# Kernel tuning notes

Measured on AMD Instinct MI355X. Metric: run time of the kernel, lower is better.

The kernel has to match this reference:

```python
import jax, jax.numpy as jnp
import numpy as np

PC_RANGE = (0.0, -40.0, -3.0, 70.4, 40.0, 1.0)
N, C, M, L = 200000, 64, 50000, 2000000
H = W = 176  # bev grid bound for synthetic pillar indices


def setup_inputs() -> dict:
    key = jax.random.key(0)
    k1, k2, k3, k4, k5, k6 = jax.random.split(key, 6)
    # points live in relative coords in [0, range_extent)
    ext = jnp.array([PC_RANGE[3] - PC_RANGE[0], PC_RANGE[4] - PC_RANGE[1], PC_RANGE[5] - PC_RANGE[2]], jnp.float32)
    xyz = jax.random.uniform(k1, (N, 3), jnp.float32) * ext
    point_features = jax.random.normal(k2, (N, C), jnp.float32)
    pillar_centers = jax.random.uniform(k3, (M, 3), jnp.float32) * ext
    pillar_indices = jax.random.randint(k4, (M, 3), 0, H, jnp.int32)
    point_set_indices = jax.random.randint(k5, (L,), 0, N, jnp.int32)
    pillar_set_indices = jnp.sort(jax.random.randint(k6, (L,), 0, M, jnp.int32))
    return {
        "xyz": xyz,
        "point_features": point_features,
        "pillar_centers": pillar_centers,
        "pillar_indices": pillar_indices,
        "point_set_indices": point_set_indices,
        "pillar_set_indices": pillar_set_indices,
    }


def reference(xyz, point_features, pillar_centers, pillar_indices, point_set_indices, pillar_set_indices):
    # gather per-pair features / coords
    group_point_features = jnp.take(point_features, point_set_indices, axis=0)   # (L, C)
    group_point_xyz = jnp.take(xyz, point_set_indices, axis=0)                   # (L, 3)
    group_pillar_centers = jnp.take(pillar_centers, pillar_set_indices, axis=0)  # (L, 3)
    # offset of each point from its pillar center (relative coords)
    rel = group_point_xyz - group_pillar_centers                                 # (L, 3)
    # shift point coords to absolute frame
    offset = jnp.array([PC_RANGE[0], PC_RANGE[1], PC_RANGE[2]], group_point_xyz.dtype)
    absl = group_point_xyz + offset                                              # (L, 3)
    group_features = jnp.concatenate([group_point_features, absl, rel], axis=1)  # (L, C+6)
    indice2bev = jnp.ones((1,), jnp.float32)  # bev_flag=False path
    return pillar_indices, pillar_set_indices, group_features, indice2bev
```

## Files before the change

kernel.cpp:

```cpp
#include <hip/hip_runtime.h>

constexpr int       kM = 50000;
constexpr long long kL = 2000000;
constexpr int       kRowLen = 70;

constexpr long long kOutPillarIdx = 0;
constexpr long long kOutPsi       = 150000;
constexpr long long kOutGF        = 2150000;
constexpr long long kOutBev       = 142150000;

constexpr int kRowsPerWave = 16;
constexpr int kWaves       = 4;
constexpr int kTileRows    = kRowsPerWave * kWaves;
constexpr int kGrid        = (int)(kL / kTileRows);
constexpr int kPillarIdx4  = kM * 3 / 4;

__global__ __launch_bounds__(256, 8)
void pillar_group_fused_kernel(const float* __restrict__ xyz,
                               const float4* __restrict__ pf4,
                               const float* __restrict__ pc,
                               const int4*  __restrict__ pillar_idx4,
                               const int4*  __restrict__ psi4,
                               const int*   __restrict__ point_set_idx,
                               const int*   __restrict__ pillar_set_idx,
                               float* __restrict__ out) {
    const int tid  = threadIdx.x;
    const int wave = tid >> 6;
    const int lane = tid & 63;
    const int row0 = blockIdx.x * kTileRows + wave * kRowsPerWave;

    if (tid < 16) {
        int k = blockIdx.x * 16 + tid;
        int4 v = psi4[k];
        ((float4*)(out + kOutPsi))[k] =
            make_float4((float)v.x, (float)v.y, (float)v.z, (float)v.w);
    } else if (tid == 16) {
        int k = blockIdx.x;
        if (k < kPillarIdx4) {
            int4 v = pillar_idx4[k];
            ((float4*)(out + kOutPillarIdx))[k] =
                make_float4((float)v.x, (float)v.y, (float)v.z, (float)v.w);
        }
    } else if (tid == 17) {
        int k = kGrid + blockIdx.x;
        if (k < kPillarIdx4) {
            int4 v = pillar_idx4[k];
            ((float4*)(out + kOutPillarIdx))[k] =
                make_float4((float)v.x, (float)v.y, (float)v.z, (float)v.w);
        }
    } else if (tid == 18 && blockIdx.x == 0) {
        out[kOutBev] = 1.0f;
    }

    int idxv = 0;
    if (lane < 16)       idxv = point_set_idx[row0 + lane];
    else if (lane < 32)  idxv = pillar_set_idx[row0 + lane - 16];

    float* gf = out + kOutGF;

    {
        const int j    = lane & 15;
        const int rsub = lane >> 4;
        #pragma unroll
        for (int it = 0; it < 4; ++it) {
            const int r = it * 4 + rsub;
            const int p = __shfl(idxv, r);
            const float4 v = pf4[(long long)p * 16 + j];
            float* dst = gf + (long long)(row0 + r) * kRowLen + j * 4;
            *(float2*)(dst)     = make_float2(v.x, v.y);
            *(float2*)(dst + 2) = make_float2(v.z, v.w);
        }
    }

    if (lane < kRowsPerWave * 3) {
        const int r = lane / 3;
        const int c = lane - r * 3;
        const int p = __shfl(idxv, r);
        const int q = __shfl(idxv, 16 + r);
        const float x   = xyz[(long long)p * 3 + c];
        const float pcv = pc[(long long)q * 3 + c];
        const float off = (c == 0) ? 0.0f : ((c == 1) ? -40.0f : -3.0f);
        float* rowp = gf + (long long)(row0 + r) * kRowLen;
        rowp[64 + c] = x + off;
        rowp[67 + c] = x - pcv;
    }
}

extern "C" void kernel_launch(void* const* d_in, const int* in_sizes, int n_in,
                              void* d_out, int out_size, void* d_ws, size_t ws_size,
                              hipStream_t stream) {
    const float* xyz             = (const float*)d_in[0];
    const float* point_features  = (const float*)d_in[1];
    const float* pillar_centers  = (const float*)d_in[2];
    const int*   pillar_indices  = (const int*)d_in[3];
    const int*   point_set_idx   = (const int*)d_in[4];
    const int*   pillar_set_idx  = (const int*)d_in[5];

    float* out = (float*)d_out;

    pillar_group_fused_kernel<<<kGrid, 256, 0, stream>>>(
        xyz, (const float4*)point_features, pillar_centers,
        (const int4*)pillar_indices, (const int4*)pillar_set_idx,
        point_set_idx, pillar_set_idx, out);
}
```

Before: 238.2 us.

## Stage gathered rows in LDS via direct global-to-LDS loads, then store as float4

Point-feature rows are now gathered straight into shared memory with global_load_lds, and the xyz/rel columns are written to LDS as well. Each wave then writes its 16x70 output tile as contiguous 16-byte stores instead of scattered float2 and scalar stores. The aim is fully coalesced, aligned wide writes on a store-bound kernel. In exchange it adds LDS usage, a full vmcnt wait, and per-element index arithmetic (division by 280) during the write-out.

```diff
diff --git a/kernel.cpp b/kernel.cpp
--- a/kernel.cpp
+++ b/kernel.cpp
@@ -15,6 +15,17 @@
 constexpr int kGrid        = (int)(kL / kTileRows);
 constexpr int kPillarIdx4  = kM * 3 / 4;
 
+constexpr int kAFloats    = kRowsPerWave * 64;
+constexpr int kBFloats    = kRowsPerWave * 6;
+constexpr int kWaveFloats = kAFloats + kBFloats;
+
+__device__ __forceinline__ void gload_lds16(const void* g, void* l) {
+    __builtin_amdgcn_global_load_lds(
+        (__attribute__((address_space(1))) void*)g,
+        (__attribute__((address_space(3))) void*)l,
+        16, 0, 0);
+}
+
 __global__ __launch_bounds__(256, 8)
 void pillar_group_fused_kernel(const float* __restrict__ xyz,
                                const float4* __restrict__ pf4,
@@ -24,10 +35,29 @@
                                const int*   __restrict__ point_set_idx,
                                const int*   __restrict__ pillar_set_idx,
                                float* __restrict__ out) {
+    __shared__ float s[kWaves * kWaveFloats];
+
     const int tid  = threadIdx.x;
     const int wave = tid >> 6;
     const int lane = tid & 63;
     const int row0 = blockIdx.x * kTileRows + wave * kRowsPerWave;
+    float* sA = &s[wave * kWaveFloats];
+    float* sB = sA + kAFloats;
+
+    int idxv = 0;
+    if (lane < 16)       idxv = point_set_idx[row0 + lane];
+    else if (lane < 32)  idxv = pillar_set_idx[row0 + lane - 16];
+
+    {
+        const int j    = lane & 15;
+        const int rsub = lane >> 4;
+        #pragma unroll
+        for (int it = 0; it < 4; ++it) {
+            const int r = it * 4 + rsub;
+            const int p = __shfl(idxv, r);
+            gload_lds16(&pf4[(long long)p * 16 + j], sA + it * 256);
+        }
+    }
 
     if (tid < 16) {
         int k = blockIdx.x * 16 + tid;
@@ -52,26 +82,6 @@
         out[kOutBev] = 1.0f;
     }
 
-    int idxv = 0;
-    if (lane < 16)       idxv = point_set_idx[row0 + lane];
-    else if (lane < 32)  idxv = pillar_set_idx[row0 + lane - 16];
-
-    float* gf = out + kOutGF;
-
-    {
-        const int j    = lane & 15;
-        const int rsub = lane >> 4;
-        #pragma unroll
-        for (int it = 0; it < 4; ++it) {
-            const int r = it * 4 + rsub;
-            const int p = __shfl(idxv, r);
-            const float4 v = pf4[(long long)p * 16 + j];
-            float* dst = gf + (long long)(row0 + r) * kRowLen + j * 4;
-            *(float2*)(dst)     = make_float2(v.x, v.y);
-            *(float2*)(dst + 2) = make_float2(v.z, v.w);
-        }
-    }
-
     if (lane < kRowsPerWave * 3) {
         const int r = lane / 3;
         const int c = lane - r * 3;
@@ -80,9 +90,32 @@
         const float x   = xyz[(long long)p * 3 + c];
         const float pcv = pc[(long long)q * 3 + c];
         const float off = (c == 0) ? 0.0f : ((c == 1) ? -40.0f : -3.0f);
-        float* rowp = gf + (long long)(row0 + r) * kRowLen;
-        rowp[64 + c] = x + off;
-        rowp[67 + c] = x - pcv;
+        sB[r * 6 + c]     = x + off;
+        sB[r * 6 + 3 + c] = x - pcv;
+    }
+
+    asm volatile("s_waitcnt vmcnt(0)" ::: "memory");
+    __builtin_amdgcn_sched_barrier(0);
+
+    {
+        const float2* A2 = (const float2*)sA;
+        const float2* B2 = (const float2*)sB;
+        float4* o4 = (float4*)(out + kOutGF + (long long)row0 * kRowLen);
+        #pragma unroll
+        for (int it = 0; it < 5; ++it) {
+            const int k = it * 64 + lane;
+            if (k < kRowsPerWave * kRowLen / 4) {
+                const unsigned b0 = (unsigned)k * 16u;
+                const unsigned b1 = b0 + 8u;
+                const unsigned r0 = b0 / 280u, o0 = b0 - r0 * 280u;
+                const unsigned r1 = b1 / 280u, o1 = b1 - r1 * 280u;
+                const float2 g0 = (o0 < 256u) ? A2[r0 * 32 + (o0 >> 3)]
+                                              : B2[r0 * 3 + ((o0 - 256u) >> 3)];
+                const float2 g1 = (o1 < 256u) ? A2[r1 * 32 + (o1 >> 3)]
+                                              : B2[r1 * 3 + ((o1 - 256u) >> 3)];
+                o4[k] = make_float4(g0.x, g0.y, g1.x, g1.y);
+            }
+        }
     }
 }
 
```

Measured after the change: 197.8 us. -17.0%, faster.
